# Performance work log

Measured on AMD Instinct MI355X. Metric: run time of the kernel, lower is better.

The kernel has to match this reference:

```python
import jax, jax.numpy as jnp
import numpy as np

N_NODES = 100000
N_EDGES = 1000000
IN_F = 64
OUT_F = 64
N_REL = 32
N_BASES = 30


def setup_inputs() -> dict:
    key = jax.random.key(0)
    k = jax.random.split(key, 8)
    node_features = jax.random.normal(k[0], (N_NODES, IN_F), dtype=jnp.float32)
    senders = jax.random.randint(k[1], (N_EDGES,), 0, N_NODES, dtype=jnp.int32)
    receivers = jax.random.randint(k[2], (N_EDGES,), 0, N_NODES, dtype=jnp.int32)
    relation_types = jax.random.randint(k[3], (N_EDGES,), 0, N_REL, dtype=jnp.int32)
    basis = jax.random.normal(k[4], (N_BASES, IN_F, OUT_F), dtype=jnp.float32) * 0.01
    coeff = jax.random.normal(k[5], (N_REL, N_BASES), dtype=jnp.float32) * 0.01
    self_weight = jax.random.normal(k[6], (IN_F, OUT_F), dtype=jnp.float32) * 0.01
    bias = jnp.zeros((OUT_F,), dtype=jnp.float32)
    return {
        "node_features": node_features,
        "senders": senders,
        "receivers": receivers,
        "relation_types": relation_types,
        "basis": basis,
        "coeff": coeff,
        "self_weight": self_weight,
        "bias": bias,
    }


def reference(node_features, senders, receivers, relation_types, basis, coeff, self_weight, bias):
    # R-GCN with basis decomposition: W_r = sum_b coeff[r,b] * basis[b].
    # The original loops over relations, masking edges; by linearity this equals
    # segment-summing source features per (receiver, relation) pair and then
    # contracting once with the relation weights -- same math, single pass.
    num_nodes = node_features.shape[0]
    n_edges = senders.shape[0]

    rel_weights = jnp.einsum('rb,bio->rio', coeff, basis)        # (R, in, out)
    src_features = node_features[senders]                         # (E, in)

    # segment id = receiver * R + relation -> (N*R, in) aggregate
    seg_ids = receivers * N_REL + relation_types
    agg = jax.ops.segment_sum(src_features, seg_ids, num_segments=num_nodes * N_REL)
    agg = agg.reshape(num_nodes, N_REL, node_features.shape[1])   # (N, R, in)

    aggregated = jnp.einsum('nri,rio->no', agg, rel_weights)      # (N, out)

    ones = jnp.ones((n_edges,), dtype=node_features.dtype)
    in_degree = jax.ops.segment_sum(ones, receivers, num_segments=num_nodes)
    in_degree = jnp.maximum(in_degree, 1.0)

    out = aggregated / in_degree[:, None]
    out = out + node_features @ self_weight
    out = out + bias
    return out
```

## Files before the change

### kernel.cpp

```cpp
#include <hip/hip_runtime.h>

#define N_F     64
#define N_REL   32
#define BLOCK   256
#define SCAN_TILE 2048

typedef __attribute__((ext_vector_type(8))) short bf16x8;
typedef __attribute__((ext_vector_type(4))) float f32x4;

__device__ __forceinline__ unsigned short f2bf(float f) {
    unsigned u = __float_as_uint(f);
    u += 0x7FFF + ((u >> 16) & 1);
    return (unsigned short)(u >> 16);
}

__global__ void __launch_bounds__(BLOCK) k_pre(const float* __restrict__ nf,
                                               const int* __restrict__ rel,
                                               const int* __restrict__ rcv,
                                               const float* __restrict__ basis,
                                               const float* __restrict__ coeff,
                                               unsigned short* __restrict__ xbf,
                                               unsigned short* __restrict__ Wsh,
                                               int* __restrict__ S,
                                               int E, int total4, int N, int nbh,
                                               int nbCast, int nbRelw) {
    const int bid = blockIdx.x;
    if (bid < nbCast) {
        int i = bid * BLOCK + threadIdx.x;
        if (i < total4) {
            float4 v = ((const float4*)nf)[i];
            ushort4 o;
            o.x = f2bf(v.x); o.y = f2bf(v.y); o.z = f2bf(v.z); o.w = f2bf(v.w);
            ((ushort4*)xbf)[i] = o;
        }
    } else if (bid < nbCast + nbRelw) {
        int idx = (bid - nbCast) * BLOCK + threadIdx.x;
        if (idx < N_REL * N_F * N_F) {
            int r  = idx >> 12;
            int io = idx & 4095;
            int k  = io >> 6;
            int n  = io & 63;
            float acc = 0.f;
#pragma unroll
            for (int b = 0; b < 30; ++b)
                acc += coeff[r * 30 + b] * basis[b * (N_F * N_F) + io];
            int ks = k >> 5, kk = k & 31;
            int nt = n >> 4, nl = n & 15;
            int lane = ((kk >> 3) << 4) | nl;
            int j    = kk & 7;
            Wsh[((((r * 2 + ks) * 4 + nt) * 64 + lane) << 3) + j] = f2bf(acc);
        }
    } else {
        __shared__ int h[N_REL];
        if (threadIdx.x < N_REL) h[threadIdx.x] = 0;
        __syncthreads();
        const int bidh = bid - nbCast - nbRelw;
        int e = bidh * BLOCK + threadIdx.x;
        if (e < E) {
            atomicAdd(&h[rel[e]], 1);
            atomicAdd(&S[rcv[e]], 1);
        }
        __syncthreads();
        if (threadIdx.x < N_REL)
            S[N + threadIdx.x * nbh + bidh] = h[threadIdx.x];
    }
}

__global__ void k_scan_sums(const int* __restrict__ cur, int* __restrict__ part,
                            int* __restrict__ cnt1,
                            int nbins, int npart, int N, int nbh) {
    __shared__ int red[BLOCK];
    const int bid = blockIdx.x;
    if (bid >= npart) {
        const int r = bid - npart;
        const int* row = cur + N + (size_t)r * nbh;
        int s = 0;
        for (int i = threadIdx.x; i < nbh; i += BLOCK) s += row[i];
        red[threadIdx.x] = s;
        __syncthreads();
        for (int off = BLOCK / 2; off > 0; off >>= 1) {
            if (threadIdx.x < off) red[threadIdx.x] += red[threadIdx.x + off];
            __syncthreads();
        }
        if (threadIdx.x == 0) cnt1[r] = red[0];
        return;
    }
    int base = bid * SCAN_TILE;
    int s = 0;
    for (int i = threadIdx.x; i < SCAN_TILE; i += BLOCK) {
        int idx = base + i;
        s += (idx < nbins) ? cur[idx] : 0;
    }
    red[threadIdx.x] = s;
    __syncthreads();
    for (int off = BLOCK / 2; off > 0; off >>= 1) {
        if (threadIdx.x < off) red[threadIdx.x] += red[threadIdx.x + off];
        __syncthreads();
    }
    if (threadIdx.x == 0) part[bid] = red[0];
}

__global__ void k_scan_mid(const int* __restrict__ cnt1, int* __restrict__ base1,
                           int* __restrict__ ub1, int* __restrict__ part,
                           int* __restrict__ esrc, int* __restrict__ perm,
                           int npart, int Ppad) {
    __shared__ int buf[BLOCK];
    __shared__ int scnt[N_REL];
    __shared__ int sbase[N_REL + 1];
    __shared__ int stotal;
    const int tid = threadIdx.x;

    if (tid < N_REL) scnt[tid] = cnt1[tid];

    int v = (tid < npart) ? part[tid] : 0;
    buf[tid] = v;
    __syncthreads();
    for (int off = 1; off < BLOCK; off <<= 1) {
        int t = (tid >= off) ? buf[tid - off] : 0;
        __syncthreads();
        buf[tid] += t;
        __syncthreads();
    }
    if (tid < npart) part[tid] = buf[tid] - v;

    if (tid == 0) {
        int acc = 0, uacc = 0;
        for (int r = 0; r < N_REL; ++r) {
            base1[r] = acc;
            sbase[r] = acc;
            ub1[r]   = uacc;
            acc  += (scnt[r] + 15) & ~15;
            uacc += scnt[r];
        }
        base1[N_REL] = Ppad;
        sbase[N_REL] = Ppad;
        ub1[N_REL]   = uacc;
        stotal = acc;
    }
    __syncthreads();

    for (int i = tid; i < N_REL * 16; i += BLOCK) {
        int r = i >> 4, o = i & 15;
        int c  = scnt[r];
        int p0 = sbase[r] + c;
        int p1 = sbase[r] + ((c + 15) & ~15);
        int p  = p0 + o;
        if (p < p1) { perm[p] = -1; esrc[p] = 0; }
    }
    for (int p = stotal + tid; p < Ppad; p += BLOCK) {
        perm[p] = -1; esrc[p] = 0;
    }
}

__global__ void k_scan_apply_tile(int* __restrict__ cur, const int* __restrict__ part,
                                  const int* __restrict__ base1,
                                  unsigned char* __restrict__ trel,
                                  int nbins, int npart, int T) {
    if ((int)blockIdx.x >= npart) {
        int t = (blockIdx.x - npart) * BLOCK + threadIdx.x;
        if (t < T) {
            int p = t << 4;
            int r = 0;
#pragma unroll
            for (int i = 1; i < N_REL; ++i) r += (p >= base1[i]);
            trel[t] = (unsigned char)r;
        }
        return;
    }
    __shared__ int buf[BLOCK];
    int base_t = blockIdx.x * SCAN_TILE + threadIdx.x * 8;
    int loc[8];
    int s = 0;
#pragma unroll
    for (int j = 0; j < 8; ++j) {
        int idx = base_t + j;
        int v = (idx < nbins) ? cur[idx] : 0;
        loc[j] = s;
        s += v;
    }
    buf[threadIdx.x] = s;
    __syncthreads();
    for (int off = 1; off < BLOCK; off <<= 1) {
        int t = (threadIdx.x >= off) ? buf[threadIdx.x - off] : 0;
        __syncthreads();
        buf[threadIdx.x] += t;
        __syncthreads();
    }
    int excl = buf[threadIdx.x] - s + part[blockIdx.x];
#pragma unroll
    for (int j = 0; j < 8; ++j) {
        int idx = base_t + j;
        if (idx < nbins) cur[idx] = loc[j] + excl;
    }
}

__global__ void __launch_bounds__(BLOCK) k_scatter1(const int* __restrict__ snd,
                                                    const int* __restrict__ rcv,
                                                    const int* __restrict__ rel,
                                                    int* S,
                                                    const int* __restrict__ base1,
                                                    const int* __restrict__ ub1,
                                                    int* __restrict__ esrc,
                                                    int* __restrict__ perm,
                                                    int E, int N, int nbh) {
    __shared__ int h[N_REL], bhb[N_REL];
    const int b = blockIdx.x;
    if (threadIdx.x < N_REL) {
        int g = S[N + threadIdx.x * nbh + b];
        bhb[threadIdx.x] = base1[threadIdx.x] + (g - E - ub1[threadIdx.x]);
        h[threadIdx.x] = 0;
    }
    __syncthreads();
    int e = b * BLOCK + threadIdx.x;
    if (e < E) {
        int r = rel[e];
        int rank = atomicAdd(&h[r], 1);
        int pos1 = bhb[r] + rank;
        int pos2 = atomicAdd(&S[rcv[e]], 1);
        esrc[pos1] = snd[e];
        perm[pos1] = pos2;
    }
}

__global__ void __launch_bounds__(BLOCK) k_gemm(const unsigned short* __restrict__ xbf,
                                                const int* __restrict__ esrc,
                                                const int* __restrict__ perm,
                                                const unsigned char* __restrict__ trel,
                                                const unsigned short* __restrict__ Wsh,
                                                unsigned short* __restrict__ eoutb,
                                                int T, int tpw, int dumprow) {
    __shared__ float ts[4][16 * 68];
    const int tid  = threadIdx.x;
    const int lane = tid & 63;
    const int wave = tid >> 6;
    float* tb = ts[wave];

    const int gw = blockIdx.x * 4 + wave;
    const int t0 = gw * tpw;
    const int t1 = min(t0 + tpw, T);
    if (t0 >= T) return;

    const int row = lane & 15;
    const int kg  = lane >> 4;
    const int rr  = lane >> 2;
    const int ch  = lane & 3;

    int curR = -1;
    bf16x8 wf[2][4];

    int s_cur  = esrc[(t0 << 4) + row];
    int pm_cur = perm[(t0 << 4) + row];

    for (int t = t0; t < t1; ++t) {
        int s_nxt = 0, pm_nxt = -1;
        if (t + 1 < t1) {
            s_nxt  = esrc[((t + 1) << 4) + row];
            pm_nxt = perm[((t + 1) << 4) + row];
        }

        const int r = trel[t];
        if (r != curR) {
            curR = r;
#pragma unroll
            for (int ks = 0; ks < 2; ++ks)
#pragma unroll
                for (int nt = 0; nt < 4; ++nt)
                    wf[ks][nt] = *(const bf16x8*)(Wsh + ((((r * 2 + ks) * 4 + nt) * 64 + lane) << 3));
        }

        const size_t xb = ((size_t)s_cur << 6) + (kg << 3);
        bf16x8 a0 = *(const bf16x8*)(xbf + xb);
        bf16x8 a1 = *(const bf16x8*)(xbf + xb + 32);

        f32x4 acc[4];
#pragma unroll
        for (int nt = 0; nt < 4; ++nt) {
            acc[nt] = (f32x4){0.f, 0.f, 0.f, 0.f};
            acc[nt] = __builtin_amdgcn_mfma_f32_16x16x32_bf16(a0, wf[0][nt], acc[nt], 0, 0, 0);
            acc[nt] = __builtin_amdgcn_mfma_f32_16x16x32_bf16(a1, wf[1][nt], acc[nt], 0, 0, 0);
        }

#pragma unroll
        for (int nt = 0; nt < 4; ++nt)
#pragma unroll
            for (int reg = 0; reg < 4; ++reg)
                tb[(kg * 4 + reg) * 68 + nt * 16 + (lane & 15)] = acc[nt][reg];

        asm volatile("s_waitcnt lgkmcnt(0)" ::: "memory");

        int pmr = __shfl(pm_cur, rr);
        pmr = (pmr < 0) ? dumprow : pmr;

        const float* src = tb + rr * 68 + ch * 16;
        unsigned pk[8];
#pragma unroll
        for (int q = 0; q < 4; ++q) {
            float4 v = *(const float4*)(src + q * 4);
            pk[2 * q]     = (unsigned)f2bf(v.x) | ((unsigned)f2bf(v.y) << 16);
            pk[2 * q + 1] = (unsigned)f2bf(v.z) | ((unsigned)f2bf(v.w) << 16);
        }
        unsigned short* dst = eoutb + (size_t)pmr * 64 + ch * 16;
        uint4 v0; v0.x = pk[0]; v0.y = pk[1]; v0.z = pk[2]; v0.w = pk[3];
        uint4 v1; v1.x = pk[4]; v1.y = pk[5]; v1.z = pk[6]; v1.w = pk[7];
        *(uint4*)dst       = v0;
        *(uint4*)(dst + 8) = v1;

        s_cur = s_nxt; pm_cur = pm_nxt;
    }
}

__global__ void __launch_bounds__(BLOCK) k_recv(const unsigned short* __restrict__ xbf,
                                                const unsigned short* __restrict__ eoutb,
                                                const int* __restrict__ cur2,
                                                const float* __restrict__ selfw,
                                                const float* __restrict__ bias,
                                                float* __restrict__ out,
                                                int N, int rpw) {
    const int tid  = threadIdx.x;
    const int lane = tid & 63;
    const int wave = tid >> 6;
    const int gw   = blockIdx.x * 4 + wave;
    const int n0   = gw * rpw;
    const int n1   = min(n0 + rpw, N);
    if (n0 >= N) return;

    const int g = lane >> 5;
    const int c = lane & 31;

    float swcol[N_F];
#pragma unroll
    for (int i = 0; i < N_F; ++i) swcol[i] = selfw[i * N_F + lane];
    const float bv = bias[lane];

    int bidx = n0 - 1 + lane;
    int bnd  = 0;
    if (bidx >= 0 && bidx < N && lane <= (n1 - n0)) bnd = cur2[bidx];

    for (int n = n0; n < n1; ++n) {
        const int li = n - n0;
        const int st = __shfl(bnd, li);
        const int en = __shfl(bnd, li + 1);

        float a0 = 0.f, a1 = 0.f;
        int j = st;
        for (; j + 8 <= en; j += 8) {
            unsigned u0 = *(const unsigned*)(eoutb + ((size_t)(j + g)     << 6) + (c << 1));
            unsigned u1 = *(const unsigned*)(eoutb + ((size_t)(j + 2 + g) << 6) + (c << 1));
            unsigned u2 = *(const unsigned*)(eoutb + ((size_t)(j + 4 + g) << 6) + (c << 1));
            unsigned u3 = *(const unsigned*)(eoutb + ((size_t)(j + 6 + g) << 6) + (c << 1));
            a0 += (__uint_as_float(u0 << 16) + __uint_as_float(u1 << 16)) +
                  (__uint_as_float(u2 << 16) + __uint_as_float(u3 << 16));
            a1 += (__uint_as_float(u0 & 0xFFFF0000u) + __uint_as_float(u1 & 0xFFFF0000u)) +
                  (__uint_as_float(u2 & 0xFFFF0000u) + __uint_as_float(u3 & 0xFFFF0000u));
        }
        if (j + 4 <= en) {
            unsigned u0 = *(const unsigned*)(eoutb + ((size_t)(j + g)     << 6) + (c << 1));
            unsigned u1 = *(const unsigned*)(eoutb + ((size_t)(j + 2 + g) << 6) + (c << 1));
            a0 += __uint_as_float(u0 << 16) + __uint_as_float(u1 << 16);
            a1 += __uint_as_float(u0 & 0xFFFF0000u) + __uint_as_float(u1 & 0xFFFF0000u);
            j += 4;
        }
        for (; j < en; j += 2) {
            int row = j + g;
            unsigned u = *(const unsigned*)(eoutb + ((size_t)row << 6) + (c << 1));
            if (row < en) {
                a0 += __uint_as_float(u << 16);
                a1 += __uint_as_float(u & 0xFFFF0000u);
            }
        }
        a0 += __shfl_xor(a0, 32);
        a1 += __shfl_xor(a1, 32);
        float v0 = __shfl(a0, lane >> 1);
        float v1 = __shfl(a1, lane >> 1);
        float agg = (lane & 1) ? v1 : v0;

        const uint4* xr = (const uint4*)(xbf + ((size_t)n << 6));
        float s0 = 0.f, s1 = 0.f, s2 = 0.f, s3 = 0.f;
#pragma unroll
        for (int q = 0; q < 8; ++q) {
            uint4 u = xr[q];
            float x0 = __uint_as_float(u.x << 16);
            float x1 = __uint_as_float(u.x & 0xFFFF0000u);
            float x2 = __uint_as_float(u.y << 16);
            float x3 = __uint_as_float(u.y & 0xFFFF0000u);
            float x4 = __uint_as_float(u.z << 16);
            float x5 = __uint_as_float(u.z & 0xFFFF0000u);
            float x6 = __uint_as_float(u.w << 16);
            float x7 = __uint_as_float(u.w & 0xFFFF0000u);
            s0 = __builtin_fmaf(x0, swcol[8 * q + 0], s0);
            s1 = __builtin_fmaf(x1, swcol[8 * q + 1], s1);
            s2 = __builtin_fmaf(x2, swcol[8 * q + 2], s2);
            s3 = __builtin_fmaf(x3, swcol[8 * q + 3], s3);
            s0 = __builtin_fmaf(x4, swcol[8 * q + 4], s0);
            s1 = __builtin_fmaf(x5, swcol[8 * q + 5], s1);
            s2 = __builtin_fmaf(x6, swcol[8 * q + 6], s2);
            s3 = __builtin_fmaf(x7, swcol[8 * q + 7], s3);
        }

        float dg  = (float)(en - st);
        float inv = 1.f / (dg < 1.f ? 1.f : dg);
        out[(size_t)n * N_F + lane] = agg * inv + (s0 + s1) + (s2 + s3) + bv;
    }
}

extern "C" void kernel_launch(void* const* d_in, const int* in_sizes, int n_in,
                              void* d_out, int out_size, void* d_ws, size_t ws_size,
                              hipStream_t stream) {
    const float* nf    = (const float*)d_in[0];
    const int*   snd   = (const int*)  d_in[1];
    const int*   rcv   = (const int*)  d_in[2];
    const int*   rel   = (const int*)  d_in[3];
    const float* basis = (const float*)d_in[4];
    const float* coeff = (const float*)d_in[5];
    const float* selfw = (const float*)d_in[6];
    const float* bias  = (const float*)d_in[7];
    float*       out   = (float*)d_out;

    const int N = in_sizes[0] / N_F;
    const int E = in_sizes[1];
    const int Ppad = (E + N_REL * 15 + 15) & ~15;
    const int T    = Ppad >> 4;
    const int total4 = N * N_F / 4;

    const int NB_CAST = (total4 + BLOCK - 1) / BLOCK;
    const int NB_RELW = (N_REL * N_F * N_F + BLOCK - 1) / BLOCK;
    const int NB_HIST = (E + BLOCK - 1) / BLOCK;
    const int nbh     = NB_HIST;

    const int SCAN_N = N + N_REL * nbh;
    const int NPART  = (SCAN_N + SCAN_TILE - 1) / SCAN_TILE;

    unsigned short* eoutb = (unsigned short*)d_ws;
    unsigned short* Wsh   = eoutb + (size_t)Ppad * N_F;
    unsigned short* xbf   = Wsh + (size_t)N_REL * N_F * N_F;
    int* base1 = (int*)(xbf + (size_t)N * N_F);
    int* ub1   = base1 + 64;
    int* cnt1  = ub1 + 64;
    int* part  = cnt1 + 32;
    int* S     = part + 256;
    int* esrc  = S + SCAN_N;
    int* perm  = esrc + Ppad;
    unsigned char* trel = (unsigned char*)(perm + Ppad);

    hipMemsetAsync(S, 0, (size_t)SCAN_N * sizeof(int), stream);

    k_pre<<<NB_CAST + NB_RELW + NB_HIST, BLOCK, 0, stream>>>(
        nf, rel, rcv, basis, coeff, xbf, Wsh, S, E, total4, N, nbh, NB_CAST, NB_RELW);

    k_scan_sums<<<NPART + N_REL, BLOCK, 0, stream>>>(S, part, cnt1, SCAN_N, NPART, N, nbh);
    k_scan_mid <<<1, BLOCK, 0, stream>>>(cnt1, base1, ub1, part, esrc, perm, NPART, Ppad);

    const int NB_TREL = (T + BLOCK - 1) / BLOCK;
    k_scan_apply_tile<<<NPART + NB_TREL, BLOCK, 0, stream>>>(S, part, base1, trel,
                                                             SCAN_N, NPART, T);

    k_scatter1<<<nbh, BLOCK, 0, stream>>>(snd, rcv, rel, S, base1, ub1, esrc, perm,
                                          E, N, nbh);

    const int GEMM_BLOCKS = 2048;
    const int tpw = (T + GEMM_BLOCKS * 4 - 1) / (GEMM_BLOCKS * 4);
    k_gemm<<<GEMM_BLOCKS, BLOCK, 0, stream>>>(xbf, esrc, perm, trel, Wsh, eoutb, T, tpw, E);

    const int RECV_BLOCKS = 4096;
    const int rpw = (N + RECV_BLOCKS * 4 - 1) / (RECV_BLOCKS * 4);
    k_recv<<<RECV_BLOCKS, BLOCK, 0, stream>>>(xbf, eoutb, S, selfw, bias, out, N, rpw);
}
```

Before: 299.6 us.

## Move self-loop GEMM into prologue kernel and vectorize receiver reduction

The self-weight product plus bias is now computed in the prologue cast blocks, in fp32 from the original features, and written to the output early. The receiver kernel then only reduces the per-edge messages and does a read-modify-write add into the output. Its reduction is restructured so that each wave handles 8 nodes, with 8 lanes per node each loading 16-byte chunks, instead of one node at a time with 4-byte loads. This shortens the critical-path receiver kernel and raises load width, at the cost of an extra output read and write and a heavier prologue.

```diff
diff --git a/kernel.cpp b/kernel.cpp
--- a/kernel.cpp
+++ b/kernel.cpp
@@ -19,19 +19,44 @@
                                                const int* __restrict__ rcv,
                                                const float* __restrict__ basis,
                                                const float* __restrict__ coeff,
+                                               const float* __restrict__ selfw,
+                                               const float* __restrict__ bias,
                                                unsigned short* __restrict__ xbf,
                                                unsigned short* __restrict__ Wsh,
+                                               float* __restrict__ out,
                                                int* __restrict__ S,
-                                               int E, int total4, int N, int nbh,
+                                               int E, int N, int nbh,
                                                int nbCast, int nbRelw) {
     const int bid = blockIdx.x;
     if (bid < nbCast) {
-        int i = bid * BLOCK + threadIdx.x;
-        if (i < total4) {
-            float4 v = ((const float4*)nf)[i];
+        const int nb0 = bid * 64;
+        const int len = min(64, N - nb0);
+        const float4* src = (const float4*)(nf + (size_t)nb0 * N_F);
+        ushort4* dst = (ushort4*)(xbf + (size_t)nb0 * N_F);
+        for (int i = threadIdx.x; i < len * 16; i += BLOCK) {
+            float4 v = src[i];
             ushort4 o;
             o.x = f2bf(v.x); o.y = f2bf(v.y); o.z = f2bf(v.z); o.w = f2bf(v.w);
-            ((ushort4*)xbf)[i] = o;
+            dst[i] = o;
+        }
+        const int lane = threadIdx.x & 63;
+        const int wave = threadIdx.x >> 6;
+        float swcol[N_F];
+#pragma unroll
+        for (int i = 0; i < N_F; ++i) swcol[i] = selfw[i * N_F + lane];
+        const float bv = bias[lane];
+        for (int nl = wave; nl < len; nl += 4) {
+            const float4* xr = (const float4*)(nf + (size_t)(nb0 + nl) * N_F);
+            float s0 = 0.f, s1 = 0.f, s2 = 0.f, s3 = 0.f;
+#pragma unroll
+            for (int q = 0; q < 16; ++q) {
+                float4 xv = xr[q];
+                s0 = __builtin_fmaf(xv.x, swcol[4 * q + 0], s0);
+                s1 = __builtin_fmaf(xv.y, swcol[4 * q + 1], s1);
+                s2 = __builtin_fmaf(xv.z, swcol[4 * q + 2], s2);
+                s3 = __builtin_fmaf(xv.w, swcol[4 * q + 3], s3);
+            }
+            out[(size_t)(nb0 + nl) * N_F + lane] = (s0 + s1) + (s2 + s3) + bv;
         }
     } else if (bid < nbCast + nbRelw) {
         int idx = (bid - nbCast) * BLOCK + threadIdx.x;
@@ -309,97 +334,76 @@
     }
 }
 
-__global__ void __launch_bounds__(BLOCK) k_recv(const unsigned short* __restrict__ xbf,
-                                                const unsigned short* __restrict__ eoutb,
+__global__ void __launch_bounds__(BLOCK) k_recv(const unsigned short* __restrict__ eoutb,
                                                 const int* __restrict__ cur2,
-                                                const float* __restrict__ selfw,
-                                                const float* __restrict__ bias,
                                                 float* __restrict__ out,
-                                                int N, int rpw) {
-    const int tid  = threadIdx.x;
-    const int lane = tid & 63;
-    const int wave = tid >> 6;
-    const int gw   = blockIdx.x * 4 + wave;
-    const int n0   = gw * rpw;
-    const int n1   = min(n0 + rpw, N);
-    if (n0 >= N) return;
-
-    const int g = lane >> 5;
-    const int c = lane & 31;
-
-    float swcol[N_F];
-#pragma unroll
-    for (int i = 0; i < N_F; ++i) swcol[i] = selfw[i * N_F + lane];
-    const float bv = bias[lane];
-
-    int bidx = n0 - 1 + lane;
+                                                int N) {
+    const int lane = threadIdx.x & 63;
+    const int wave = threadIdx.x >> 6;
+    const int nb   = (blockIdx.x * 4 + wave) * 8;
+    if (nb >= N) return;
+
+    const int sub = lane >> 3;
+    const int c   = lane & 7;
+
+    int bidx = nb - 1 + lane;
     int bnd  = 0;
-    if (bidx >= 0 && bidx < N && lane <= (n1 - n0)) bnd = cur2[bidx];
-
-    for (int n = n0; n < n1; ++n) {
-        const int li = n - n0;
-        const int st = __shfl(bnd, li);
-        const int en = __shfl(bnd, li + 1);
-
-        float a0 = 0.f, a1 = 0.f;
-        int j = st;
-        for (; j + 8 <= en; j += 8) {
-            unsigned u0 = *(const unsigned*)(eoutb + ((size_t)(j + g)     << 6) + (c << 1));
-            unsigned u1 = *(const unsigned*)(eoutb + ((size_t)(j + 2 + g) << 6) + (c << 1));
-            unsigned u2 = *(const unsigned*)(eoutb + ((size_t)(j + 4 + g) << 6) + (c << 1));
-            unsigned u3 = *(const unsigned*)(eoutb + ((size_t)(j + 6 + g) << 6) + (c << 1));
-            a0 += (__uint_as_float(u0 << 16) + __uint_as_float(u1 << 16)) +
-                  (__uint_as_float(u2 << 16) + __uint_as_float(u3 << 16));
-            a1 += (__uint_as_float(u0 & 0xFFFF0000u) + __uint_as_float(u1 & 0xFFFF0000u)) +
-                  (__uint_as_float(u2 & 0xFFFF0000u) + __uint_as_float(u3 & 0xFFFF0000u));
-        }
-        if (j + 4 <= en) {
-            unsigned u0 = *(const unsigned*)(eoutb + ((size_t)(j + g)     << 6) + (c << 1));
-            unsigned u1 = *(const unsigned*)(eoutb + ((size_t)(j + 2 + g) << 6) + (c << 1));
-            a0 += __uint_as_float(u0 << 16) + __uint_as_float(u1 << 16);
-            a1 += __uint_as_float(u0 & 0xFFFF0000u) + __uint_as_float(u1 & 0xFFFF0000u);
-            j += 4;
-        }
-        for (; j < en; j += 2) {
-            int row = j + g;
-            unsigned u = *(const unsigned*)(eoutb + ((size_t)row << 6) + (c << 1));
-            if (row < en) {
-                a0 += __uint_as_float(u << 16);
-                a1 += __uint_as_float(u & 0xFFFF0000u);
-            }
-        }
-        a0 += __shfl_xor(a0, 32);
-        a1 += __shfl_xor(a1, 32);
-        float v0 = __shfl(a0, lane >> 1);
-        float v1 = __shfl(a1, lane >> 1);
-        float agg = (lane & 1) ? v1 : v0;
-
-        const uint4* xr = (const uint4*)(xbf + ((size_t)n << 6));
-        float s0 = 0.f, s1 = 0.f, s2 = 0.f, s3 = 0.f;
-#pragma unroll
-        for (int q = 0; q < 8; ++q) {
-            uint4 u = xr[q];
-            float x0 = __uint_as_float(u.x << 16);
-            float x1 = __uint_as_float(u.x & 0xFFFF0000u);
-            float x2 = __uint_as_float(u.y << 16);
-            float x3 = __uint_as_float(u.y & 0xFFFF0000u);
-            float x4 = __uint_as_float(u.z << 16);
-            float x5 = __uint_as_float(u.z & 0xFFFF0000u);
-            float x6 = __uint_as_float(u.w << 16);
-            float x7 = __uint_as_float(u.w & 0xFFFF0000u);
-            s0 = __builtin_fmaf(x0, swcol[8 * q + 0], s0);
-            s1 = __builtin_fmaf(x1, swcol[8 * q + 1], s1);
-            s2 = __builtin_fmaf(x2, swcol[8 * q + 2], s2);
-            s3 = __builtin_fmaf(x3, swcol[8 * q + 3], s3);
-            s0 = __builtin_fmaf(x4, swcol[8 * q + 4], s0);
-            s1 = __builtin_fmaf(x5, swcol[8 * q + 5], s1);
-            s2 = __builtin_fmaf(x6, swcol[8 * q + 6], s2);
-            s3 = __builtin_fmaf(x7, swcol[8 * q + 7], s3);
-        }
-
+    if (lane <= 8 && bidx >= 0 && bidx < N) bnd = cur2[bidx];
+    int st = __shfl(bnd, sub);
+    int en = __shfl(bnd, sub + 1);
+    const int n = nb + sub;
+    if (n >= N) { st = 0; en = 0; }
+
+    float a[8];
+#pragma unroll
+    for (int i = 0; i < 8; ++i) a[i] = 0.f;
+
+    const uint4* ep = (const uint4*)eoutb;
+    int j = st;
+    for (; j + 4 <= en; j += 4) {
+        uint4 u0 = ep[(size_t)(j + 0) * 8 + c];
+        uint4 u1 = ep[(size_t)(j + 1) * 8 + c];
+        uint4 u2 = ep[(size_t)(j + 2) * 8 + c];
+        uint4 u3 = ep[(size_t)(j + 3) * 8 + c];
+        a[0] += (__uint_as_float(u0.x << 16) + __uint_as_float(u1.x << 16)) +
+                (__uint_as_float(u2.x << 16) + __uint_as_float(u3.x << 16));
+        a[1] += (__uint_as_float(u0.x & 0xFFFF0000u) + __uint_as_float(u1.x & 0xFFFF0000u)) +
+                (__uint_as_float(u2.x & 0xFFFF0000u) + __uint_as_float(u3.x & 0xFFFF0000u));
+        a[2] += (__uint_as_float(u0.y << 16) + __uint_as_float(u1.y << 16)) +
+                (__uint_as_float(u2.y << 16) + __uint_as_float(u3.y << 16));
+        a[3] += (__uint_as_float(u0.y & 0xFFFF0000u) + __uint_as_float(u1.y & 0xFFFF0000u)) +
+                (__uint_as_float(u2.y & 0xFFFF0000u) + __uint_as_float(u3.y & 0xFFFF0000u));
+        a[4] += (__uint_as_float(u0.z << 16) + __uint_as_float(u1.z << 16)) +
+                (__uint_as_float(u2.z << 16) + __uint_as_float(u3.z << 16));
+        a[5] += (__uint_as_float(u0.z & 0xFFFF0000u) + __uint_as_float(u1.z & 0xFFFF0000u)) +
+                (__uint_as_float(u2.z & 0xFFFF0000u) + __uint_as_float(u3.z & 0xFFFF0000u));
+        a[6] += (__uint_as_float(u0.w << 16) + __uint_as_float(u1.w << 16)) +
+                (__uint_as_float(u2.w << 16) + __uint_as_float(u3.w << 16));
+        a[7] += (__uint_as_float(u0.w & 0xFFFF0000u) + __uint_as_float(u1.w & 0xFFFF0000u)) +
+                (__uint_as_float(u2.w & 0xFFFF0000u) + __uint_as_float(u3.w & 0xFFFF0000u));
+    }
+    for (; j < en; ++j) {
+        uint4 u0 = ep[(size_t)j * 8 + c];
+        a[0] += __uint_as_float(u0.x << 16);
+        a[1] += __uint_as_float(u0.x & 0xFFFF0000u);
+        a[2] += __uint_as_float(u0.y << 16);
+        a[3] += __uint_as_float(u0.y & 0xFFFF0000u);
+        a[4] += __uint_as_float(u0.z << 16);
+        a[5] += __uint_as_float(u0.z & 0xFFFF0000u);
+        a[6] += __uint_as_float(u0.w << 16);
+        a[7] += __uint_as_float(u0.w & 0xFFFF0000u);
+    }
+
+    if (n < N) {
         float dg  = (float)(en - st);
         float inv = 1.f / (dg < 1.f ? 1.f : dg);
-        out[(size_t)n * N_F + lane] = agg * inv + (s0 + s1) + (s2 + s3) + bv;
+        float* op = out + (size_t)n * N_F + c * 8;
+        float4 p0 = *(const float4*)op;
+        float4 p1 = *(const float4*)(op + 4);
+        p0.x += a[0] * inv; p0.y += a[1] * inv; p0.z += a[2] * inv; p0.w += a[3] * inv;
+        p1.x += a[4] * inv; p1.y += a[5] * inv; p1.z += a[6] * inv; p1.w += a[7] * inv;
+        *(float4*)op       = p0;
+        *(float4*)(op + 4) = p1;
     }
 }
 
@@ -420,9 +424,8 @@
     const int E = in_sizes[1];
     const int Ppad = (E + N_REL * 15 + 15) & ~15;
     const int T    = Ppad >> 4;
-    const int total4 = N * N_F / 4;
-
-    const int NB_CAST = (total4 + BLOCK - 1) / BLOCK;
+
+    const int NB_CAST = (N + 63) / 64;
     const int NB_RELW = (N_REL * N_F * N_F + BLOCK - 1) / BLOCK;
     const int NB_HIST = (E + BLOCK - 1) / BLOCK;
     const int nbh     = NB_HIST;
@@ -445,7 +448,8 @@
     hipMemsetAsync(S, 0, (size_t)SCAN_N * sizeof(int), stream);
 
     k_pre<<<NB_CAST + NB_RELW + NB_HIST, BLOCK, 0, stream>>>(
-        nf, rel, rcv, basis, coeff, xbf, Wsh, S, E, total4, N, nbh, NB_CAST, NB_RELW);
+        nf, rel, rcv, basis, coeff, selfw, bias, xbf, Wsh, out, S,
+        E, N, nbh, NB_CAST, NB_RELW);
 
     k_scan_sums<<<NPART + N_REL, BLOCK, 0, stream>>>(S, part, cnt1, SCAN_N, NPART, N, nbh);
     k_scan_mid <<<1, BLOCK, 0, stream>>>(cnt1, base1, ub1, part, esrc, perm, NPART, Ppad);
@@ -461,7 +465,6 @@
     const int tpw = (T + GEMM_BLOCKS * 4 - 1) / (GEMM_BLOCKS * 4);
     k_gemm<<<GEMM_BLOCKS, BLOCK, 0, stream>>>(xbf, esrc, perm, trel, Wsh, eoutb, T, tpw, E);
 
-    const int RECV_BLOCKS = 4096;
-    const int rpw = (N + RECV_BLOCKS * 4 - 1) / (RECV_BLOCKS * 4);
-    k_recv<<<RECV_BLOCKS, BLOCK, 0, stream>>>(xbf, eoutb, S, selfw, bias, out, N, rpw);
-}
+    const int RECV_BLOCKS = (N + 31) / 32;
+    k_recv<<<RECV_BLOCKS, BLOCK, 0, stream>>>(eoutb, S, out, N);
+}
```

New measurement: 317.0 us. 5.8% more time.
